# Performance work log

Measured on AMD Instinct MI355X. Metric: run time of the kernel, lower is better.

The kernel has to match this reference:

```python
import jax, jax.numpy as jnp
import numpy as np

RING_SIZES = list(range(3, 27, 2))  # 3,5,...,25 -> 12 rings; (1+12)*96 = 1248
BN_EPS = 1e-5


def _box_sum(x, k):
    """Sum over k x k window (k odd), 'same' zero padding. x: [B,C,H,W].
    O(1) per pixel via summed-area table instead of dense depthwise conv."""
    p = k // 2
    H, W = x.shape[2], x.shape[3]
    xp = jnp.pad(x, ((0, 0), (0, 0), (p, p), (p, p)))
    S = jnp.cumsum(jnp.cumsum(xp, axis=2), axis=3)
    S = jnp.pad(S, ((0, 0), (0, 0), (1, 0), (1, 0)))  # leading zero row/col
    return (S[:, :, k:k + H, k:k + W] - S[:, :, :H, k:k + W]
            - S[:, :, k:k + H, :W] + S[:, :, :H, :W])


def _ring_sum(x, k):
    """Depthwise conv with a k x k ring of ones == box(k) - box(k-2)."""
    inner = x if k == 3 else _box_sum(x, k - 2)
    return _box_sum(x, k) - inner


def _bn_eval(x, gamma, beta, mean, var):
    scale = gamma / jnp.sqrt(var + BN_EPS)
    return x * scale[None, :, None, None] + (beta - mean * scale)[None, :, None, None]


def _conv1x1(x, w, b):
    # x: [B,C,H,W], w: [O,C] -> [B,O,H,W]
    return jnp.einsum('bchw,oc->bohw', x, w) + b[None, :, None, None]


def setup_inputs() -> dict:
    key = jax.random.key(0)
    ks = jax.random.split(key, 13)
    B, C, H, W = 4, 96, 128, 128
    return {
        'x': jax.random.normal(ks[0], (B, C, H, W), jnp.float32),
        'bn1_gamma': jax.random.uniform(ks[1], (1248,), jnp.float32, 0.5, 1.5),
        'bn1_beta': jax.random.normal(ks[2], (1248,), jnp.float32) * 0.1,
        'bn1_mean': jax.random.normal(ks[3], (1248,), jnp.float32),
        'bn1_var': jax.random.uniform(ks[4], (1248,), jnp.float32, 0.5, 1.5),
        'conv1_w': jax.random.normal(ks[5], (512, 1248), jnp.float32) * (1.0 / np.sqrt(1248)),
        'conv1_b': jax.random.normal(ks[6], (512,), jnp.float32) * 0.01,
        'bn2_gamma': jax.random.uniform(ks[7], (512,), jnp.float32, 0.5, 1.5),
        'bn2_beta': jax.random.normal(ks[8], (512,), jnp.float32) * 0.1,
        'bn2_mean': jax.random.normal(ks[9], (512,), jnp.float32),
        'bn2_var': jax.random.uniform(ks[10], (512,), jnp.float32, 0.5, 1.5),
        'conv2_w': jax.random.normal(ks[11], (96, 512), jnp.float32) * (1.0 / np.sqrt(512)),
        'conv2_b': jax.random.normal(ks[12], (96,), jnp.float32) * 0.01,
    }


def reference(x, bn1_gamma, bn1_beta, bn1_mean, bn1_var, conv1_w, conv1_b,
              bn2_gamma, bn2_beta, bn2_mean, bn2_var, conv2_w, conv2_b):
    convs = [x] + [_ring_sum(x, k) for k in RING_SIZES]
    h = jnp.concatenate(convs, axis=1)  # [B, 1248, H, W]
    h = _bn_eval(h, bn1_gamma, bn1_beta, bn1_mean, bn1_var)
    h = jax.nn.relu(_conv1x1(h, conv1_w, conv1_b))
    h = _bn_eval(h, bn2_gamma, bn2_beta, bn2_mean, bn2_var)
    return _conv1x1(h, conv2_w, conv2_b)
```

## Files before the change

### kernel.cpp

```cpp
#include <hip/hip_runtime.h>
#include <hip/hip_bf16.h>
#include <cstdint>

typedef __attribute__((ext_vector_type(8))) short bf16x8;
typedef __attribute__((ext_vector_type(4))) float f32x4;

#define BN_EPS 1e-5f

__global__ __launch_bounds__(256) void prep1_kernel(
    const float* __restrict__ W1, const float* __restrict__ cb1,
    const float* __restrict__ g1, const float* __restrict__ be1,
    const float* __restrict__ mu1, const float* __restrict__ va1,
    __hip_bfloat16* __restrict__ V, float* __restrict__ b1e)
{
  int o = blockIdx.x;
  int t = threadIdx.x;
  const float* wrow = W1 + (size_t)o * 1248;
  float acc = 0.f;
  for (int i = t; i < 1248; i += 256) {
    float s = g1[i] * rsqrtf(va1[i] + BN_EPS);
    float w = wrow[i];
    acc += w * (be1[i] - mu1[i] * s);
    float g = w * s;
    float gn = 0.f;
    if (i < 1152) {
      float sn = g1[i + 96] * rsqrtf(va1[i + 96] + BN_EPS);
      gn = wrow[i + 96] * sn;
    }
    V[(size_t)o * 1248 + i] = __float2bfloat16(g - gn);
  }
  for (int d = 32; d > 0; d >>= 1) acc += __shfl_down(acc, d);
  __shared__ float red[4];
  int lane = t & 63, wv = t >> 6;
  if (lane == 0) red[wv] = acc;
  __syncthreads();
  if (t == 0) b1e[o] = cb1[o] + red[0] + red[1] + red[2] + red[3];
}

__global__ __launch_bounds__(256) void prep2_kernel(
    const float* __restrict__ W2, const float* __restrict__ cb2,
    const float* __restrict__ g2, const float* __restrict__ be2,
    const float* __restrict__ mu2, const float* __restrict__ va2,
    __hip_bfloat16* __restrict__ W2e, float* __restrict__ b2e)
{
  int o = blockIdx.x;
  int t = threadIdx.x;
  const float* wrow = W2 + (size_t)o * 512;
  float acc = 0.f;
  for (int j = t; j < 512; j += 256) {
    float s = g2[j] * rsqrtf(va2[j] + BN_EPS);
    float wv = wrow[j];
    acc += wv * (be2[j] - mu2[j] * s);
    W2e[(size_t)o * 512 + j] = __float2bfloat16(wv * s);
  }
  for (int d = 32; d > 0; d >>= 1) acc += __shfl_down(acc, d);
  __shared__ float red[4];
  int lane = t & 63, wv2 = t >> 6;
  if (lane == 0) red[wv2] = acc;
  __syncthreads();
  if (t == 0) b2e[o] = cb2[o] + red[0] + red[1] + red[2] + red[3];
}

__global__ __launch_bounds__(512) void sat_kernel(
    const float* __restrict__ x, float* __restrict__ SAT)
{
  int plane = blockIdx.x;
  const float* xp = x + (size_t)plane * 16384;
  __shared__ float tile[16384];
  __shared__ float csA[128 * 4];
  __shared__ float csB[128 * 4];
  int t = threadIdx.x;

  for (int i4 = t; i4 < 4096; i4 += 512) {
    int r = i4 >> 5;
    int g = i4 & 31;
    float4 v = *(const float4*)(xp + (size_t)r * 128 + g * 4);
    *(float4*)(tile + r * 128 + ((g ^ (r & 31)) << 2)) = v;
  }
  __syncthreads();

  int r = t & 127, ch = t >> 7;
  {
    float carry = 0.f;
#pragma unroll
    for (int g8 = 0; g8 < 8; ++g8) {
      int g = ch * 8 + g8;
      float* p = tile + r * 128 + ((g ^ (r & 31)) << 2);
      float4 v = *(float4*)p;
      float s0 = carry + v.x, s1 = s0 + v.y, s2 = s1 + v.z, s3 = s2 + v.w;
      float4 o; o.x = s0; o.y = s1; o.z = s2; o.w = s3;
      *(float4*)p = o;
      carry = s3;
    }
    csA[r * 4 + ch] = carry;
  }
  __syncthreads();
  if (ch > 0) {
    float offs = csA[r * 4 + 0];
    if (ch > 1) offs += csA[r * 4 + 1];
    if (ch > 2) offs += csA[r * 4 + 2];
#pragma unroll
    for (int g8 = 0; g8 < 8; ++g8) {
      int g = ch * 8 + g8;
      float* p = tile + r * 128 + ((g ^ (r & 31)) << 2);
      float4 v = *(float4*)p;
      v.x += offs; v.y += offs; v.z += offs; v.w += offs;
      *(float4*)p = v;
    }
  }
  __syncthreads();

  float* Sg = SAT + (size_t)plane * 17028;
  int xcol = t & 127, rc = t >> 7;
  int gc = xcol >> 2, wc = xcol & 3;
  float regs[32];
  {
    float run = 0.f;
#pragma unroll
    for (int r8 = 0; r8 < 32; ++r8) {
      int rr = rc * 32 + r8;
      run += tile[rr * 128 + ((gc ^ (rr & 31)) << 2) + wc];
      regs[r8] = run;
    }
    csB[xcol * 4 + rc] = run;
  }
  if (t < 132) Sg[t] = 0.f;
  if (t < 128) Sg[(t + 1) * 132] = 0.f;
  __syncthreads();

  float offs = 0.f;
  if (rc > 0) offs += csB[xcol * 4 + 0];
  if (rc > 1) offs += csB[xcol * 4 + 1];
  if (rc > 2) offs += csB[xcol * 4 + 2];
#pragma unroll
  for (int r8 = 0; r8 < 32; ++r8) {
    int rr = rc * 32 + r8;
    Sg[(rr + 1) * 132 + xcol + 1] = regs[r8] + offs;
  }
}

__global__ __launch_bounds__(1024) void fused1_kernel(
    const float* __restrict__ SAT, const __hip_bfloat16* __restrict__ V,
    const float* __restrict__ b1e, const __hip_bfloat16* __restrict__ W2e,
    const float* __restrict__ b2e, float* __restrict__ out, int nb, int b0)
{
  extern __shared__ __align__(16) char smem[];
  float* E0 = (float*)smem;
  float* E1 = (float*)(smem + 50688);
  __hip_bfloat16* As0 = (__hip_bfloat16*)(smem + 101376);
  __hip_bfloat16* As1 = (__hip_bfloat16*)(smem + 128000);

  int blk = blockIdx.x;
  int rows_per_xcd = (nb * 128) >> 3;
  int r = (blk & 7) * rows_per_xcd + (blk >> 3);
  int bL = r >> 7, y = r & 127;

  int t = threadIdx.x;
  int lane = t & 63, wv = t >> 6;
  int wm = wv & 1, wn = wv >> 1;
  int lr = lane & 15, quad = lane >> 4;
  int px = t & 127;
  int bg = t >> 7;

  const float* Sb = SAT + (size_t)bL * 96 * 17028;

  f32x4 acc[4][4];
#pragma unroll
  for (int i = 0; i < 4; ++i)
#pragma unroll
    for (int jn = 0; jn < 4; ++jn) acc[i][jn] = (f32x4){0.f, 0.f, 0.f, 0.f};

  auto efill = [&](float* E, int jr) {
    int y1 = (y - jr < 0) ? 0 : (y - jr);
    int y2 = ((y + jr > 127) ? 127 : (y + jr)) + 1;
    for (int idx = t; idx < 3168; idx += 1024) {
      int cl = idx / 33;
      int ck = idx - cl * 33;
      const float* bp = Sb + (size_t)cl * 17028 + ck * 4;
      float4 a = *(const float4*)(bp + y2 * 132);
      float4 b = *(const float4*)(bp + y1 * 132);
      float4 d;
      d.x = a.x - b.x; d.y = a.y - b.y; d.z = a.z - b.z; d.w = a.w - b.w;
      *(float4*)(E + cl * 132 + ck * 4) = d;
    }
  };

  auto build = [&](__hip_bfloat16* As, const float* E, int jr) {
    int x1 = (px - jr < 0) ? 0 : (px - jr);
    int x2 = ((px + jr > 127) ? 127 : (px + jr)) + 1;
    const float* Eb = E + bg * 8 * 132;
    union { bf16x8 v; __hip_bfloat16 h[8]; } pk;
#pragma unroll
    for (int i = 0; i < 8; ++i)
      pk.h[i] = __float2bfloat16(Eb[i * 132 + x2] - Eb[i * 132 + x1]);
    *(bf16x8*)(As + px * 104 + bg * 8) = pk.v;
    if (bg < 4) {
      const float* Eb2 = E + (8 + bg) * 8 * 132;
      union { bf16x8 v; __hip_bfloat16 h[8]; } pk2;
#pragma unroll
      for (int i = 0; i < 8; ++i)
        pk2.h[i] = __float2bfloat16(Eb2[i * 132 + x2] - Eb2[i * 132 + x1]);
      *(bf16x8*)(As + px * 104 + (8 + bg) * 8) = pk2.v;
    }
  };

  auto mfma_ring = [&](int j, const __hip_bfloat16* As) {
    __builtin_amdgcn_s_setprio(1);
#pragma unroll
    for (int sub = 0; sub < 3; ++sub) {
      bf16x8 af[4], bfr[4];
#pragma unroll
      for (int i = 0; i < 4; ++i)
        af[i] = *(const bf16x8*)(As + (wm * 64 + i * 16 + lr) * 104 + sub * 32 + quad * 8);
#pragma unroll
      for (int jn = 0; jn < 4; ++jn)
        bfr[jn] = *(const bf16x8*)(V + (size_t)(wn * 64 + jn * 16 + lr) * 1248
                                   + j * 96 + sub * 32 + quad * 8);
#pragma unroll
      for (int i = 0; i < 4; ++i)
#pragma unroll
        for (int jn = 0; jn < 4; ++jn)
          acc[i][jn] = __builtin_amdgcn_mfma_f32_16x16x32_bf16(af[i], bfr[jn], acc[i][jn], 0, 0, 0);
    }
    __builtin_amdgcn_s_setprio(0);
  };

  auto ring_iter = [&](int j, const float* Esrc, float* Edst,
                       const __hip_bfloat16* Asrc, __hip_bfloat16* Adst) {
    if (wv & 1) {
      mfma_ring(j, Asrc);
      if (j < 11) efill(Edst, j + 2);
      if (j < 12) build(Adst, Esrc, j + 1);
    } else {
      if (j < 11) efill(Edst, j + 2);
      if (j < 12) build(Adst, Esrc, j + 1);
      mfma_ring(j, Asrc);
    }
    __syncthreads();
  };

  efill(E0, 0);
  __syncthreads();
  efill(E1, 1);
  build(As0, E0, 0);
  __syncthreads();

  for (int j = 0; j < 13; j += 2) {
    ring_iter(j, E1, E0, As0, As1);
    if (j + 1 < 13) ring_iter(j + 1, E0, E1, As1, As0);
  }

  __hip_bfloat16* Yst = (__hip_bfloat16*)smem;
#pragma unroll
  for (int jn = 0; jn < 4; ++jn) {
    int n = wn * 64 + jn * 16 + lr;
    float bias = b1e[n];
#pragma unroll
    for (int i = 0; i < 4; ++i) {
#pragma unroll
      for (int rr = 0; rr < 4; ++rr) {
        int m = wm * 64 + i * 16 + quad * 4 + rr;
        float z = acc[i][jn][rr] + bias;
        z = z > 0.f ? z : 0.f;
        Yst[m * 520 + n] = __float2bfloat16(z);
      }
    }
  }
  __syncthreads();

  int pxt = wv & 7;
  int mh = wv >> 3;
  f32x4 acc2[3];
#pragma unroll
  for (int im = 0; im < 3; ++im) acc2[im] = (f32x4){0.f, 0.f, 0.f, 0.f};

  for (int k2 = 0; k2 < 512; k2 += 32) {
    bf16x8 bfr2 = *(const bf16x8*)(Yst + (pxt * 16 + lr) * 520 + k2 + quad * 8);
#pragma unroll
    for (int im = 0; im < 3; ++im) {
      bf16x8 afr2 = *(const bf16x8*)(W2e + (size_t)(mh * 48 + im * 16 + lr) * 512
                                     + k2 + quad * 8);
      acc2[im] = __builtin_amdgcn_mfma_f32_16x16x32_bf16(afr2, bfr2, acc2[im], 0, 0, 0);
    }
  }

  size_t obase = ((size_t)(b0 + bL) * 96) * 16384 + (size_t)y * 128 + pxt * 16 + lr;
#pragma unroll
  for (int im = 0; im < 3; ++im) {
#pragma unroll
    for (int rr = 0; rr < 4; ++rr) {
      int o2 = mh * 48 + im * 16 + quad * 4 + rr;
      out[obase + (size_t)o2 * 16384] = acc2[im][rr] + b2e[o2];
    }
  }
}

extern "C" void kernel_launch(void* const* d_in, const int* in_sizes, int n_in,
                              void* d_out, int out_size, void* d_ws, size_t ws_size,
                              hipStream_t stream)
{
  const float* x   = (const float*)d_in[0];
  const float* g1  = (const float*)d_in[1];
  const float* be1 = (const float*)d_in[2];
  const float* mu1 = (const float*)d_in[3];
  const float* va1 = (const float*)d_in[4];
  const float* W1  = (const float*)d_in[5];
  const float* cb1 = (const float*)d_in[6];
  const float* g2  = (const float*)d_in[7];
  const float* be2 = (const float*)d_in[8];
  const float* mu2 = (const float*)d_in[9];
  const float* va2 = (const float*)d_in[10];
  const float* W2  = (const float*)d_in[11];
  const float* cb2 = (const float*)d_in[12];
  float* out = (float*)d_out;

  hipFuncSetAttribute((const void*)fused1_kernel,
                      hipFuncAttributeMaxDynamicSharedMemorySize, 154624);

  char* w = (char*)d_ws;
  __hip_bfloat16* V   = (__hip_bfloat16*)w; w += (size_t)512 * 1248 * 2;
  __hip_bfloat16* W2e = (__hip_bfloat16*)w; w += (size_t)96 * 512 * 2;
  float* b1e = (float*)w; w += 2048;
  float* b2e = (float*)w; w += 512;
  size_t fixed = (size_t)(w - (char*)d_ws);

  const size_t satB = (size_t)96 * 17028 * 4;
  int nb = (ws_size >= fixed + 4 * satB + 4096) ? 4 : 1;

  float* SAT = (float*)w;

  prep1_kernel<<<512, 256, 0, stream>>>(W1, cb1, g1, be1, mu1, va1, V, b1e);
  prep2_kernel<<<96, 256, 0, stream>>>(W2, cb2, g2, be2, mu2, va2, W2e, b2e);

  for (int b0 = 0; b0 < 4; b0 += nb) {
    sat_kernel<<<nb * 96, 512, 0, stream>>>(x + (size_t)b0 * 96 * 16384, SAT);
    fused1_kernel<<<nb * 128, 1024, 154624, stream>>>(SAT, V, b1e, W2e, b2e, out, nb, b0);
  }
}
```

Before: 302.4 us.

## Restructure fused kernel to 512 threads with larger per-wave tiles and register-staged prefetch

Cuts the fused kernel block from 1024 to 512 threads. Each wave now computes a 128-output by 64-pixel tile with 32 accumulators, taking A fragments from global V and B from shared memory. The double-buffered A tile is replaced by a single buffer, and SAT row differences are prefetched into registers between MFMA sub-steps, with an extra sync per ring. The aim is more register-level reuse of V fragments and better overlap of global loads with MFMA. The cost is much higher register pressure, which makes the launch_bounds(512,2) occupancy target hard to meet, plus an extra barrier per ring iteration.

```diff
diff --git a/kernel.cpp b/kernel.cpp
--- a/kernel.cpp
+++ b/kernel.cpp
@@ -3,6 +3,7 @@
 #include <cstdint>
 
 typedef __attribute__((ext_vector_type(8))) short bf16x8;
+typedef __attribute__((ext_vector_type(4))) short bf16x4;
 typedef __attribute__((ext_vector_type(4))) float f32x4;
 
 #define BN_EPS 1e-5f
@@ -139,7 +140,7 @@
   }
 }
 
-__global__ __launch_bounds__(1024) void fused1_kernel(
+__global__ __launch_bounds__(512, 2) void fused1_kernel(
     const float* __restrict__ SAT, const __hip_bfloat16* __restrict__ V,
     const float* __restrict__ b1e, const __hip_bfloat16* __restrict__ W2e,
     const float* __restrict__ b2e, float* __restrict__ out, int nb, int b0)
@@ -147,8 +148,7 @@
   extern __shared__ __align__(16) char smem[];
   float* E0 = (float*)smem;
   float* E1 = (float*)(smem + 50688);
-  __hip_bfloat16* As0 = (__hip_bfloat16*)(smem + 101376);
-  __hip_bfloat16* As1 = (__hip_bfloat16*)(smem + 128000);
+  __hip_bfloat16* As = (__hip_bfloat16*)(smem + 101376);
 
   int blk = blockIdx.x;
   int rows_per_xcd = (nb * 128) >> 3;
@@ -157,140 +157,163 @@
 
   int t = threadIdx.x;
   int lane = t & 63, wv = t >> 6;
-  int wm = wv & 1, wn = wv >> 1;
+  int wo = wv >> 1, wp = wv & 1;
   int lr = lane & 15, quad = lane >> 4;
   int px = t & 127;
   int bg = t >> 7;
 
   const float* Sb = SAT + (size_t)bL * 96 * 17028;
 
-  f32x4 acc[4][4];
-#pragma unroll
-  for (int i = 0; i < 4; ++i)
-#pragma unroll
-    for (int jn = 0; jn < 4; ++jn) acc[i][jn] = (f32x4){0.f, 0.f, 0.f, 0.f};
-
-  auto efill = [&](float* E, int jr) {
-    int y1 = (y - jr < 0) ? 0 : (y - jr);
-    int y2 = ((y + jr > 127) ? 127 : (y + jr)) + 1;
-    for (int idx = t; idx < 3168; idx += 1024) {
-      int cl = idx / 33;
-      int ck = idx - cl * 33;
+  f32x4 acc[8][4];
+#pragma unroll
+  for (int io = 0; io < 8; ++io)
+#pragma unroll
+    for (int ip = 0; ip < 4; ++ip) acc[io][ip] = (f32x4){0.f, 0.f, 0.f, 0.f};
+
+  float4 ea[3], eb[3];
+  float ta = 0.f, tb = 0.f;
+
+  auto eload = [&](int jr, int h) {
+    int y1 = ((y - jr < 0) ? 0 : (y - jr)) * 132;
+    int y2 = (((y + jr > 127) ? 127 : (y + jr)) + 1) * 132;
+#pragma unroll
+    for (int k = 0; k < 3; ++k) {
+      int idx = t + 512 * (h * 3 + k);
+      int cl = idx >> 5, ck = idx & 31;
       const float* bp = Sb + (size_t)cl * 17028 + ck * 4;
-      float4 a = *(const float4*)(bp + y2 * 132);
-      float4 b = *(const float4*)(bp + y1 * 132);
+      ea[k] = *(const float4*)(bp + y2);
+      eb[k] = *(const float4*)(bp + y1);
+    }
+    if (h == 1 && t < 96) {
+      const float* bp = Sb + (size_t)t * 17028 + 128;
+      ta = bp[y2];
+      tb = bp[y1];
+    }
+  };
+
+  auto ewrite = [&](float* E, int h) {
+#pragma unroll
+    for (int k = 0; k < 3; ++k) {
+      int idx = t + 512 * (h * 3 + k);
+      int cl = idx >> 5, ck = idx & 31;
       float4 d;
-      d.x = a.x - b.x; d.y = a.y - b.y; d.z = a.z - b.z; d.w = a.w - b.w;
+      d.x = ea[k].x - eb[k].x; d.y = ea[k].y - eb[k].y;
+      d.z = ea[k].z - eb[k].z; d.w = ea[k].w - eb[k].w;
       *(float4*)(E + cl * 132 + ck * 4) = d;
     }
+    if (h == 1 && t < 96) E[t * 132 + 128] = ta - tb;
   };
 
-  auto build = [&](__hip_bfloat16* As, const float* E, int jr) {
+  auto build = [&](const float* E, int jr) {
     int x1 = (px - jr < 0) ? 0 : (px - jr);
     int x2 = ((px + jr > 127) ? 127 : (px + jr)) + 1;
-    const float* Eb = E + bg * 8 * 132;
-    union { bf16x8 v; __hip_bfloat16 h[8]; } pk;
-#pragma unroll
-    for (int i = 0; i < 8; ++i)
-      pk.h[i] = __float2bfloat16(Eb[i * 132 + x2] - Eb[i * 132 + x1]);
-    *(bf16x8*)(As + px * 104 + bg * 8) = pk.v;
-    if (bg < 4) {
-      const float* Eb2 = E + (8 + bg) * 8 * 132;
-      union { bf16x8 v; __hip_bfloat16 h[8]; } pk2;
+#pragma unroll
+    for (int k = 0; k < 3; ++k) {
+      int g = bg + 4 * k;
+      const float* Eb = E + g * 8 * 132;
+      union { bf16x8 v; __hip_bfloat16 h[8]; } pk;
 #pragma unroll
       for (int i = 0; i < 8; ++i)
-        pk2.h[i] = __float2bfloat16(Eb2[i * 132 + x2] - Eb2[i * 132 + x1]);
-      *(bf16x8*)(As + px * 104 + (8 + bg) * 8) = pk2.v;
+        pk.h[i] = __float2bfloat16(Eb[i * 132 + x2] - Eb[i * 132 + x1]);
+      *(bf16x8*)(As + px * 104 + g * 8) = pk.v;
     }
   };
 
-  auto mfma_ring = [&](int j, const __hip_bfloat16* As) {
+  auto mfma_sub = [&](int j, int sub) {
+    bf16x8 av[8], bs[4];
+#pragma unroll
+    for (int io = 0; io < 8; ++io)
+      av[io] = *(const bf16x8*)(V + (size_t)(wo * 128 + io * 16 + lr) * 1248
+                                + j * 96 + sub * 32 + quad * 8);
+#pragma unroll
+    for (int ip = 0; ip < 4; ++ip)
+      bs[ip] = *(const bf16x8*)(As + (wp * 64 + ip * 16 + lr) * 104 + sub * 32 + quad * 8);
     __builtin_amdgcn_s_setprio(1);
 #pragma unroll
-    for (int sub = 0; sub < 3; ++sub) {
-      bf16x8 af[4], bfr[4];
-#pragma unroll
-      for (int i = 0; i < 4; ++i)
-        af[i] = *(const bf16x8*)(As + (wm * 64 + i * 16 + lr) * 104 + sub * 32 + quad * 8);
-#pragma unroll
-      for (int jn = 0; jn < 4; ++jn)
-        bfr[jn] = *(const bf16x8*)(V + (size_t)(wn * 64 + jn * 16 + lr) * 1248
-                                   + j * 96 + sub * 32 + quad * 8);
-#pragma unroll
-      for (int i = 0; i < 4; ++i)
-#pragma unroll
-        for (int jn = 0; jn < 4; ++jn)
-          acc[i][jn] = __builtin_amdgcn_mfma_f32_16x16x32_bf16(af[i], bfr[jn], acc[i][jn], 0, 0, 0);
-    }
+    for (int io = 0; io < 8; ++io)
+#pragma unroll
+      for (int ip = 0; ip < 4; ++ip)
+        acc[io][ip] = __builtin_amdgcn_mfma_f32_16x16x32_bf16(av[io], bs[ip], acc[io][ip], 0, 0, 0);
     __builtin_amdgcn_s_setprio(0);
   };
 
-  auto ring_iter = [&](int j, const float* Esrc, float* Edst,
-                       const __hip_bfloat16* Asrc, __hip_bfloat16* Adst) {
-    if (wv & 1) {
-      mfma_ring(j, Asrc);
-      if (j < 11) efill(Edst, j + 2);
-      if (j < 12) build(Adst, Esrc, j + 1);
-    } else {
-      if (j < 11) efill(Edst, j + 2);
-      if (j < 12) build(Adst, Esrc, j + 1);
-      mfma_ring(j, Asrc);
-    }
+  eload(0, 0); ewrite(E0, 0); eload(0, 1); ewrite(E0, 1);
+  __syncthreads();
+  eload(1, 0); ewrite(E1, 0); eload(1, 1);
+  build(E0, 0);
+  ewrite(E1, 1);
+  __syncthreads();
+
+  for (int j = 0; j < 13; ++j) {
+    float* EJ = (j & 1) ? E1 : E0;
+    const float* EK = (j & 1) ? E0 : E1;
+    bool pf = (j < 11);
+    if (pf) eload(j + 2, 0);
+    mfma_sub(j, 0);
+    if (pf) { ewrite(EJ, 0); eload(j + 2, 1); }
+    mfma_sub(j, 1);
+    mfma_sub(j, 2);
+    if (pf) ewrite(EJ, 1);
     __syncthreads();
-  };
-
-  efill(E0, 0);
-  __syncthreads();
-  efill(E1, 1);
-  build(As0, E0, 0);
-  __syncthreads();
-
-  for (int j = 0; j < 13; j += 2) {
-    ring_iter(j, E1, E0, As0, As1);
-    if (j + 1 < 13) ring_iter(j + 1, E0, E1, As1, As0);
+    if (j < 12) build(EK, j + 1);
+    __syncthreads();
   }
 
   __hip_bfloat16* Yst = (__hip_bfloat16*)smem;
 #pragma unroll
-  for (int jn = 0; jn < 4; ++jn) {
-    int n = wn * 64 + jn * 16 + lr;
-    float bias = b1e[n];
-#pragma unroll
-    for (int i = 0; i < 4; ++i) {
+  for (int io = 0; io < 8; ++io) {
+    int o1b = wo * 128 + io * 16 + quad * 4;
+    float4 bias = *(const float4*)(b1e + o1b);
+#pragma unroll
+    for (int ip = 0; ip < 4; ++ip) {
+      int pxx = wp * 64 + ip * 16 + lr;
+      f32x4 a = acc[io][ip];
+      float z0 = a[0] + bias.x; z0 = z0 > 0.f ? z0 : 0.f;
+      float z1 = a[1] + bias.y; z1 = z1 > 0.f ? z1 : 0.f;
+      float z2 = a[2] + bias.z; z2 = z2 > 0.f ? z2 : 0.f;
+      float z3 = a[3] + bias.w; z3 = z3 > 0.f ? z3 : 0.f;
+      union { bf16x4 v; __hip_bfloat16 h[4]; } pk;
+      pk.h[0] = __float2bfloat16(z0); pk.h[1] = __float2bfloat16(z1);
+      pk.h[2] = __float2bfloat16(z2); pk.h[3] = __float2bfloat16(z3);
+      *(bf16x4*)(Yst + pxx * 520 + o1b) = pk.v;
+    }
+  }
+  __syncthreads();
+
+  int og = wv >> 2;
+  int pg = wv & 3;
+  f32x4 acc2[3][2];
+#pragma unroll
+  for (int im = 0; im < 3; ++im)
+#pragma unroll
+    for (int tl = 0; tl < 2; ++tl) acc2[im][tl] = (f32x4){0.f, 0.f, 0.f, 0.f};
+
+  for (int k2 = 0; k2 < 512; k2 += 32) {
+    bf16x8 bfr2[2];
+#pragma unroll
+    for (int tl = 0; tl < 2; ++tl)
+      bfr2[tl] = *(const bf16x8*)(Yst + (pg * 32 + tl * 16 + lr) * 520 + k2 + quad * 8);
+#pragma unroll
+    for (int im = 0; im < 3; ++im) {
+      bf16x8 afr2 = *(const bf16x8*)(W2e + (size_t)(og * 48 + im * 16 + lr) * 512
+                                     + k2 + quad * 8);
+#pragma unroll
+      for (int tl = 0; tl < 2; ++tl)
+        acc2[im][tl] = __builtin_amdgcn_mfma_f32_16x16x32_bf16(afr2, bfr2[tl], acc2[im][tl], 0, 0, 0);
+    }
+  }
+
+  size_t obase = ((size_t)(b0 + bL) * 96) * 16384 + (size_t)y * 128;
+#pragma unroll
+  for (int im = 0; im < 3; ++im) {
+#pragma unroll
+    for (int tl = 0; tl < 2; ++tl) {
+      int pxx = pg * 32 + tl * 16 + lr;
 #pragma unroll
       for (int rr = 0; rr < 4; ++rr) {
-        int m = wm * 64 + i * 16 + quad * 4 + rr;
-        float z = acc[i][jn][rr] + bias;
-        z = z > 0.f ? z : 0.f;
-        Yst[m * 520 + n] = __float2bfloat16(z);
+        int o2 = og * 48 + im * 16 + quad * 4 + rr;
+        out[obase + (size_t)o2 * 16384 + pxx] = acc2[im][tl][rr] + b2e[o2];
       }
-    }
-  }
-  __syncthreads();
-
-  int pxt = wv & 7;
-  int mh = wv >> 3;
-  f32x4 acc2[3];
-#pragma unroll
-  for (int im = 0; im < 3; ++im) acc2[im] = (f32x4){0.f, 0.f, 0.f, 0.f};
-
-  for (int k2 = 0; k2 < 512; k2 += 32) {
-    bf16x8 bfr2 = *(const bf16x8*)(Yst + (pxt * 16 + lr) * 520 + k2 + quad * 8);
-#pragma unroll
-    for (int im = 0; im < 3; ++im) {
-      bf16x8 afr2 = *(const bf16x8*)(W2e + (size_t)(mh * 48 + im * 16 + lr) * 512
-                                     + k2 + quad * 8);
-      acc2[im] = __builtin_amdgcn_mfma_f32_16x16x32_bf16(afr2, bfr2, acc2[im], 0, 0, 0);
-    }
-  }
-
-  size_t obase = ((size_t)(b0 + bL) * 96) * 16384 + (size_t)y * 128 + pxt * 16 + lr;
-#pragma unroll
-  for (int im = 0; im < 3; ++im) {
-#pragma unroll
-    for (int rr = 0; rr < 4; ++rr) {
-      int o2 = mh * 48 + im * 16 + quad * 4 + rr;
-      out[obase + (size_t)o2 * 16384] = acc2[im][rr] + b2e[o2];
     }
   }
 }
@@ -315,7 +338,7 @@
   float* out = (float*)d_out;
 
   hipFuncSetAttribute((const void*)fused1_kernel,
-                      hipFuncAttributeMaxDynamicSharedMemorySize, 154624);
+                      hipFuncAttributeMaxDynamicSharedMemorySize, 133120);
 
   char* w = (char*)d_ws;
   __hip_bfloat16* V   = (__hip_bfloat16*)w; w += (size_t)512 * 1248 * 2;
@@ -334,6 +357,6 @@
 
   for (int b0 = 0; b0 < 4; b0 += nb) {
     sat_kernel<<<nb * 96, 512, 0, stream>>>(x + (size_t)b0 * 96 * 16384, SAT);
-    fused1_kernel<<<nb * 128, 1024, 154624, stream>>>(SAT, V, b1e, W2e, b2e, out, nb, b0);
-  }
-}
+    fused1_kernel<<<nb * 128, 512, 133120, stream>>>(SAT, V, b1e, W2e, b2e, out, nb, b0);
+  }
+}
```

New measurement: 288.9 us. 1.05x faster.

## Split fused kernel into producer/consumer waves over half-row tiles, merge prep kernels

Applied to the files above, without the earlier changes.

Merges the two weight-prep kernels and the SAT kernel into one launch. The main kernel now handles 64-pixel half-rows and uses 1024 blocks. It dedicates half the waves to producing the ring A-tile from the SAT through a small swizzled transposed LDS staging buffer, while the other half run MFMAs, with a double-buffered A tile. Shared memory drops from about 151KB to 65KB, which may let two blocks share a CU. The trade-off is more redundant SAT reads from the halo columns, and only half the waves issue MFMAs.

```diff
diff --git a/kernel.cpp b/kernel.cpp
--- a/kernel.cpp
+++ b/kernel.cpp
@@ -3,73 +3,17 @@
 #include <cstdint>
 
 typedef __attribute__((ext_vector_type(8))) short bf16x8;
+typedef __attribute__((ext_vector_type(4))) short bf16x4;
 typedef __attribute__((ext_vector_type(4))) float f32x4;
 
 #define BN_EPS 1e-5f
 
-__global__ __launch_bounds__(256) void prep1_kernel(
-    const float* __restrict__ W1, const float* __restrict__ cb1,
-    const float* __restrict__ g1, const float* __restrict__ be1,
-    const float* __restrict__ mu1, const float* __restrict__ va1,
-    __hip_bfloat16* __restrict__ V, float* __restrict__ b1e)
-{
-  int o = blockIdx.x;
-  int t = threadIdx.x;
-  const float* wrow = W1 + (size_t)o * 1248;
-  float acc = 0.f;
-  for (int i = t; i < 1248; i += 256) {
-    float s = g1[i] * rsqrtf(va1[i] + BN_EPS);
-    float w = wrow[i];
-    acc += w * (be1[i] - mu1[i] * s);
-    float g = w * s;
-    float gn = 0.f;
-    if (i < 1152) {
-      float sn = g1[i + 96] * rsqrtf(va1[i + 96] + BN_EPS);
-      gn = wrow[i + 96] * sn;
-    }
-    V[(size_t)o * 1248 + i] = __float2bfloat16(g - gn);
-  }
-  for (int d = 32; d > 0; d >>= 1) acc += __shfl_down(acc, d);
-  __shared__ float red[4];
-  int lane = t & 63, wv = t >> 6;
-  if (lane == 0) red[wv] = acc;
-  __syncthreads();
-  if (t == 0) b1e[o] = cb1[o] + red[0] + red[1] + red[2] + red[3];
-}
-
-__global__ __launch_bounds__(256) void prep2_kernel(
-    const float* __restrict__ W2, const float* __restrict__ cb2,
-    const float* __restrict__ g2, const float* __restrict__ be2,
-    const float* __restrict__ mu2, const float* __restrict__ va2,
-    __hip_bfloat16* __restrict__ W2e, float* __restrict__ b2e)
-{
-  int o = blockIdx.x;
-  int t = threadIdx.x;
-  const float* wrow = W2 + (size_t)o * 512;
-  float acc = 0.f;
-  for (int j = t; j < 512; j += 256) {
-    float s = g2[j] * rsqrtf(va2[j] + BN_EPS);
-    float wv = wrow[j];
-    acc += wv * (be2[j] - mu2[j] * s);
-    W2e[(size_t)o * 512 + j] = __float2bfloat16(wv * s);
-  }
-  for (int d = 32; d > 0; d >>= 1) acc += __shfl_down(acc, d);
-  __shared__ float red[4];
-  int lane = t & 63, wv2 = t >> 6;
-  if (lane == 0) red[wv2] = acc;
-  __syncthreads();
-  if (t == 0) b2e[o] = cb2[o] + red[0] + red[1] + red[2] + red[3];
-}
-
-__global__ __launch_bounds__(512) void sat_kernel(
-    const float* __restrict__ x, float* __restrict__ SAT)
-{
-  int plane = blockIdx.x;
-  const float* xp = x + (size_t)plane * 16384;
+__device__ __forceinline__ void sat_plane(const float* __restrict__ xp,
+                                          float* __restrict__ Sg, int t)
+{
   __shared__ float tile[16384];
-  __shared__ float csA[128 * 4];
-  __shared__ float csB[128 * 4];
-  int t = threadIdx.x;
+  __shared__ float csA[512];
+  __shared__ float csB[512];
 
   for (int i4 = t; i4 < 4096; i4 += 512) {
     int r = i4 >> 5;
@@ -110,7 +54,6 @@
   }
   __syncthreads();
 
-  float* Sg = SAT + (size_t)plane * 17028;
   int xcol = t & 127, rc = t >> 7;
   int gc = xcol >> 2, wc = xcol & 3;
   float regs[32];
@@ -126,6 +69,10 @@
   }
   if (t < 132) Sg[t] = 0.f;
   if (t < 128) Sg[(t + 1) * 132] = 0.f;
+  if (t < 128) {
+    float* rp = Sg + (size_t)(t + 1) * 132;
+    rp[129] = 0.f; rp[130] = 0.f; rp[131] = 0.f;
+  }
   __syncthreads();
 
   float offs = 0.f;
@@ -139,158 +86,246 @@
   }
 }
 
-__global__ __launch_bounds__(1024) void fused1_kernel(
+__global__ __launch_bounds__(512) void prepsat_kernel(
+    const float* __restrict__ W1, const float* __restrict__ cb1,
+    const float* __restrict__ g1, const float* __restrict__ be1,
+    const float* __restrict__ mu1, const float* __restrict__ va1,
+    const float* __restrict__ W2, const float* __restrict__ cb2,
+    const float* __restrict__ g2, const float* __restrict__ be2,
+    const float* __restrict__ mu2, const float* __restrict__ va2,
+    const float* __restrict__ x,
+    __hip_bfloat16* __restrict__ V, float* __restrict__ b1e,
+    __hip_bfloat16* __restrict__ W2e, float* __restrict__ b2e,
+    float* __restrict__ SAT, int nplanes)
+{
+  int blk = blockIdx.x;
+  int t = threadIdx.x;
+  if (blk < 512) {
+    __shared__ float red[8];
+    int o = blk;
+    const float* wrow = W1 + (size_t)o * 1248;
+    float acc = 0.f;
+    for (int i = t; i < 1248; i += 512) {
+      float s = g1[i] * rsqrtf(va1[i] + BN_EPS);
+      float w = wrow[i];
+      acc += w * (be1[i] - mu1[i] * s);
+      float g = w * s;
+      float gn = 0.f;
+      if (i < 1152) {
+        float sn = g1[i + 96] * rsqrtf(va1[i + 96] + BN_EPS);
+        gn = wrow[i + 96] * sn;
+      }
+      V[(size_t)o * 1248 + i] = __float2bfloat16(g - gn);
+    }
+    for (int d = 32; d > 0; d >>= 1) acc += __shfl_down(acc, d);
+    int lane = t & 63, wvv = t >> 6;
+    if (lane == 0) red[wvv] = acc;
+    __syncthreads();
+    if (t == 0) {
+      float s = cb1[o];
+#pragma unroll
+      for (int i = 0; i < 8; ++i) s += red[i];
+      b1e[o] = s;
+    }
+  } else if (blk < 608) {
+    __shared__ float red2[8];
+    int o = blk - 512;
+    const float* wrow = W2 + (size_t)o * 512;
+    float acc = 0.f;
+    {
+      int j = t;
+      float s = g2[j] * rsqrtf(va2[j] + BN_EPS);
+      float wv = wrow[j];
+      acc = wv * (be2[j] - mu2[j] * s);
+      W2e[(size_t)o * 512 + j] = __float2bfloat16(wv * s);
+    }
+    for (int d = 32; d > 0; d >>= 1) acc += __shfl_down(acc, d);
+    int lane = t & 63, wvv = t >> 6;
+    if (lane == 0) red2[wvv] = acc;
+    __syncthreads();
+    if (t == 0) {
+      float s = cb2[o];
+#pragma unroll
+      for (int i = 0; i < 8; ++i) s += red2[i];
+      b2e[o] = s;
+    }
+  } else {
+    int plane = blk - 608;
+    if (plane < nplanes)
+      sat_plane(x + (size_t)plane * 16384, SAT + (size_t)plane * 17028, t);
+  }
+}
+
+__global__ __launch_bounds__(512) void satonly_kernel(
+    const float* __restrict__ x, float* __restrict__ SAT)
+{
+  sat_plane(x + (size_t)blockIdx.x * 16384,
+            SAT + (size_t)blockIdx.x * 17028, threadIdx.x);
+}
+
+__global__ __launch_bounds__(1024) void fused3_kernel(
     const float* __restrict__ SAT, const __hip_bfloat16* __restrict__ V,
     const float* __restrict__ b1e, const __hip_bfloat16* __restrict__ W2e,
     const float* __restrict__ b2e, float* __restrict__ out, int nb, int b0)
 {
   extern __shared__ __align__(16) char smem[];
-  float* E0 = (float*)smem;
-  float* E1 = (float*)(smem + 50688);
-  __hip_bfloat16* As0 = (__hip_bfloat16*)(smem + 101376);
-  __hip_bfloat16* As1 = (__hip_bfloat16*)(smem + 128000);
+  float* ET = (float*)smem;
+  __hip_bfloat16* As0 = (__hip_bfloat16*)(smem + 36800);
+  __hip_bfloat16* As1 = (__hip_bfloat16*)(smem + 50112);
 
   int blk = blockIdx.x;
-  int rows_per_xcd = (nb * 128) >> 3;
-  int r = (blk & 7) * rows_per_xcd + (blk >> 3);
-  int bL = r >> 7, y = r & 127;
+  int per_xcd = (nb * 256) >> 3;
+  int r = (blk & 7) * per_xcd + (blk >> 3);
+  int bL = r >> 8;
+  int rem = r & 255;
+  int y = rem >> 1, h = rem & 1;
+  int x0 = h * 64 - 12;
+  const float* Sb = SAT + (size_t)bL * 96 * 17028;
 
   int t = threadIdx.x;
   int lane = t & 63, wv = t >> 6;
-  int wm = wv & 1, wn = wv >> 1;
   int lr = lane & 15, quad = lane >> 4;
-  int px = t & 127;
-  int bg = t >> 7;
-
-  const float* Sb = SAT + (size_t)bL * 96 * 17028;
+  bool isC = (wv & 4) != 0;
+  int role = (wv & 3) | (((wv >> 3) & 1) << 2);
 
   f32x4 acc[4][4];
 #pragma unroll
-  for (int i = 0; i < 4; ++i)
-#pragma unroll
-    for (int jn = 0; jn < 4; ++jn) acc[i][jn] = (f32x4){0.f, 0.f, 0.f, 0.f};
-
-  auto efill = [&](float* E, int jr) {
-    int y1 = (y - jr < 0) ? 0 : (y - jr);
-    int y2 = ((y + jr > 127) ? 127 : (y + jr)) + 1;
-    for (int idx = t; idx < 3168; idx += 1024) {
-      int cl = idx / 33;
-      int ck = idx - cl * 33;
-      const float* bp = Sb + (size_t)cl * 17028 + ck * 4;
-      float4 a = *(const float4*)(bp + y2 * 132);
-      float4 b = *(const float4*)(bp + y1 * 132);
-      float4 d;
-      d.x = a.x - b.x; d.y = a.y - b.y; d.z = a.z - b.z; d.w = a.w - b.w;
-      *(float4*)(E + cl * 132 + ck * 4) = d;
+  for (int io = 0; io < 4; ++io)
+#pragma unroll
+    for (int ip = 0; ip < 4; ++ip) acc[io][ip] = (f32x4){0.f, 0.f, 0.f, 0.f};
+
+  int cb = role * 12;
+  int pxl = lane;
+  int pxg = h * 64 + pxl;
+
+  auto produce = [&](__hip_bfloat16* As, int jr) {
+    int y1 = (y - jr < 0 ? 0 : y - jr) * 132;
+    int y2 = ((y + jr > 127 ? 127 : y + jr) + 1) * 132;
+#pragma unroll
+    for (int it = 0; it < 5; ++it) {
+      int idx = lane + (it << 6);
+      if (idx < 276) {
+        int clp = idx / 46;
+        int xq = idx - clp * 46;
+        int cl = cb + clp * 2;
+        int xg = x0 + (xq << 1);
+        xg = xg < 0 ? 0 : (xg > 128 ? 128 : xg);
+        const float* p0 = Sb + (size_t)cl * 17028 + xg;
+        float2 a2 = *(const float2*)(p0 + y2);
+        float2 a1 = *(const float2*)(p0 + y1);
+        float2 c2 = *(const float2*)(p0 + 17028 + y2);
+        float2 c1 = *(const float2*)(p0 + 17028 + y1);
+        int xl = xq << 1;
+        int sw = ((xl >> 3) & 7) << 2;
+        int cw = cl ^ sw;
+        *(float2*)(ET + xl * 100 + cw) = make_float2(a2.x - a1.x, c2.x - c1.x);
+        *(float2*)(ET + xl * 100 + 100 + cw) = make_float2(a2.y - a1.y, c2.y - c1.y);
+      }
+    }
+    asm volatile("s_waitcnt lgkmcnt(0)" ::: "memory");
+    __builtin_amdgcn_sched_barrier(0);
+    int x2l = ((pxg + jr > 127 ? 127 : pxg + jr) + 1) - x0;
+    int x1l = ((pxg - jr < 0 ? 0 : pxg - jr)) - x0;
+    int s2 = ((x2l >> 3) & 7) << 2;
+    int s1 = ((x1l >> 3) & 7) << 2;
+    const float* r2 = ET + x2l * 100;
+    const float* r1 = ET + x1l * 100;
+#pragma unroll
+    for (int k = 0; k < 3; ++k) {
+      int c = cb + (k << 2);
+      float4 e2 = *(const float4*)(r2 + (c ^ s2));
+      float4 e1 = *(const float4*)(r1 + (c ^ s1));
+      union { bf16x4 v; __hip_bfloat16 hh[4]; } pk;
+      pk.hh[0] = __float2bfloat16(e2.x - e1.x);
+      pk.hh[1] = __float2bfloat16(e2.y - e1.y);
+      pk.hh[2] = __float2bfloat16(e2.z - e1.z);
+      pk.hh[3] = __float2bfloat16(e2.w - e1.w);
+      *(bf16x4*)(As + pxl * 104 + c) = pk.v;
     }
   };
 
-  auto build = [&](__hip_bfloat16* As, const float* E, int jr) {
-    int x1 = (px - jr < 0) ? 0 : (px - jr);
-    int x2 = ((px + jr > 127) ? 127 : (px + jr)) + 1;
-    const float* Eb = E + bg * 8 * 132;
-    union { bf16x8 v; __hip_bfloat16 h[8]; } pk;
-#pragma unroll
-    for (int i = 0; i < 8; ++i)
-      pk.h[i] = __float2bfloat16(Eb[i * 132 + x2] - Eb[i * 132 + x1]);
-    *(bf16x8*)(As + px * 104 + bg * 8) = pk.v;
-    if (bg < 4) {
-      const float* Eb2 = E + (8 + bg) * 8 * 132;
-      union { bf16x8 v; __hip_bfloat16 h[8]; } pk2;
-#pragma unroll
-      for (int i = 0; i < 8; ++i)
-        pk2.h[i] = __float2bfloat16(Eb2[i * 132 + x2] - Eb2[i * 132 + x1]);
-      *(bf16x8*)(As + px * 104 + (8 + bg) * 8) = pk2.v;
+  const __hip_bfloat16* Vb = V + (size_t)(role * 64) * 1248;
+  auto mfma_ring = [&](int j, const __hip_bfloat16* As) {
+#pragma unroll
+    for (int sub = 0; sub < 3; ++sub) {
+      bf16x8 av[4], bs[4];
+#pragma unroll
+      for (int io = 0; io < 4; ++io)
+        av[io] = *(const bf16x8*)(Vb + (size_t)(io * 16 + lr) * 1248
+                                  + j * 96 + sub * 32 + quad * 8);
+#pragma unroll
+      for (int ip = 0; ip < 4; ++ip)
+        bs[ip] = *(const bf16x8*)(As + (ip * 16 + lr) * 104 + sub * 32 + quad * 8);
+      __builtin_amdgcn_s_setprio(1);
+#pragma unroll
+      for (int io = 0; io < 4; ++io)
+#pragma unroll
+        for (int ip = 0; ip < 4; ++ip)
+          acc[io][ip] = __builtin_amdgcn_mfma_f32_16x16x32_bf16(
+              av[io], bs[ip], acc[io][ip], 0, 0, 0);
+      __builtin_amdgcn_s_setprio(0);
     }
   };
 
-  auto mfma_ring = [&](int j, const __hip_bfloat16* As) {
-    __builtin_amdgcn_s_setprio(1);
-#pragma unroll
-    for (int sub = 0; sub < 3; ++sub) {
-      bf16x8 af[4], bfr[4];
-#pragma unroll
-      for (int i = 0; i < 4; ++i)
-        af[i] = *(const bf16x8*)(As + (wm * 64 + i * 16 + lr) * 104 + sub * 32 + quad * 8);
-#pragma unroll
-      for (int jn = 0; jn < 4; ++jn)
-        bfr[jn] = *(const bf16x8*)(V + (size_t)(wn * 64 + jn * 16 + lr) * 1248
-                                   + j * 96 + sub * 32 + quad * 8);
-#pragma unroll
-      for (int i = 0; i < 4; ++i)
-#pragma unroll
-        for (int jn = 0; jn < 4; ++jn)
-          acc[i][jn] = __builtin_amdgcn_mfma_f32_16x16x32_bf16(af[i], bfr[jn], acc[i][jn], 0, 0, 0);
-    }
-    __builtin_amdgcn_s_setprio(0);
-  };
-
-  auto ring_iter = [&](int j, const float* Esrc, float* Edst,
-                       const __hip_bfloat16* Asrc, __hip_bfloat16* Adst) {
-    if (wv & 1) {
-      mfma_ring(j, Asrc);
-      if (j < 11) efill(Edst, j + 2);
-      if (j < 12) build(Adst, Esrc, j + 1);
+  if (!isC) produce(As0, 0);
+  __syncthreads();
+
+  for (int j = 0; j < 13; ++j) {
+    if (!isC) {
+      if (j < 12) produce((j & 1) ? As0 : As1, j + 1);
     } else {
-      if (j < 11) efill(Edst, j + 2);
-      if (j < 12) build(Adst, Esrc, j + 1);
-      mfma_ring(j, Asrc);
+      mfma_ring(j, (j & 1) ? As1 : As0);
     }
     __syncthreads();
-  };
-
-  efill(E0, 0);
-  __syncthreads();
-  efill(E1, 1);
-  build(As0, E0, 0);
-  __syncthreads();
-
-  for (int j = 0; j < 13; j += 2) {
-    ring_iter(j, E1, E0, As0, As1);
-    if (j + 1 < 13) ring_iter(j + 1, E0, E1, As1, As0);
   }
 
   __hip_bfloat16* Yst = (__hip_bfloat16*)smem;
-#pragma unroll
-  for (int jn = 0; jn < 4; ++jn) {
-    int n = wn * 64 + jn * 16 + lr;
-    float bias = b1e[n];
-#pragma unroll
-    for (int i = 0; i < 4; ++i) {
+  if (isC) {
+#pragma unroll
+    for (int io = 0; io < 4; ++io) {
+      int o1b = role * 64 + io * 16 + quad * 4;
+      float4 bias = *(const float4*)(b1e + o1b);
+#pragma unroll
+      for (int ip = 0; ip < 4; ++ip) {
+        int pxx = ip * 16 + lr;
+        f32x4 a = acc[io][ip];
+        float z0 = a[0] + bias.x; z0 = z0 > 0.f ? z0 : 0.f;
+        float z1 = a[1] + bias.y; z1 = z1 > 0.f ? z1 : 0.f;
+        float z2 = a[2] + bias.z; z2 = z2 > 0.f ? z2 : 0.f;
+        float z3 = a[3] + bias.w; z3 = z3 > 0.f ? z3 : 0.f;
+        union { bf16x4 v; __hip_bfloat16 hh[4]; } pk;
+        pk.hh[0] = __float2bfloat16(z0); pk.hh[1] = __float2bfloat16(z1);
+        pk.hh[2] = __float2bfloat16(z2); pk.hh[3] = __float2bfloat16(z3);
+        *(bf16x4*)(Yst + pxx * 520 + o1b) = pk.v;
+      }
+    }
+  }
+  __syncthreads();
+
+  if (isC) {
+    int mh = role >> 2;
+    int pq = role & 3;
+    f32x4 acc2[3];
+#pragma unroll
+    for (int im = 0; im < 3; ++im) acc2[im] = (f32x4){0.f, 0.f, 0.f, 0.f};
+    for (int k2 = 0; k2 < 512; k2 += 32) {
+      bf16x8 b2f = *(const bf16x8*)(Yst + (pq * 16 + lr) * 520 + k2 + quad * 8);
+#pragma unroll
+      for (int im = 0; im < 3; ++im) {
+        bf16x8 a2f = *(const bf16x8*)(W2e + (size_t)(mh * 48 + im * 16 + lr) * 512
+                                      + k2 + quad * 8);
+        acc2[im] = __builtin_amdgcn_mfma_f32_16x16x32_bf16(a2f, b2f, acc2[im], 0, 0, 0);
+      }
+    }
+    size_t obase = ((size_t)(b0 + bL) * 96) * 16384 + (size_t)y * 128
+                   + h * 64 + pq * 16 + lr;
+#pragma unroll
+    for (int im = 0; im < 3; ++im) {
 #pragma unroll
       for (int rr = 0; rr < 4; ++rr) {
-        int m = wm * 64 + i * 16 + quad * 4 + rr;
-        float z = acc[i][jn][rr] + bias;
-        z = z > 0.f ? z : 0.f;
-        Yst[m * 520 + n] = __float2bfloat16(z);
-      }
-    }
-  }
-  __syncthreads();
-
-  int pxt = wv & 7;
-  int mh = wv >> 3;
-  f32x4 acc2[3];
-#pragma unroll
-  for (int im = 0; im < 3; ++im) acc2[im] = (f32x4){0.f, 0.f, 0.f, 0.f};
-
-  for (int k2 = 0; k2 < 512; k2 += 32) {
-    bf16x8 bfr2 = *(const bf16x8*)(Yst + (pxt * 16 + lr) * 520 + k2 + quad * 8);
-#pragma unroll
-    for (int im = 0; im < 3; ++im) {
-      bf16x8 afr2 = *(const bf16x8*)(W2e + (size_t)(mh * 48 + im * 16 + lr) * 512
-                                     + k2 + quad * 8);
-      acc2[im] = __builtin_amdgcn_mfma_f32_16x16x32_bf16(afr2, bfr2, acc2[im], 0, 0, 0);
-    }
-  }
-
-  size_t obase = ((size_t)(b0 + bL) * 96) * 16384 + (size_t)y * 128 + pxt * 16 + lr;
-#pragma unroll
-  for (int im = 0; im < 3; ++im) {
-#pragma unroll
-    for (int rr = 0; rr < 4; ++rr) {
-      int o2 = mh * 48 + im * 16 + quad * 4 + rr;
-      out[obase + (size_t)o2 * 16384] = acc2[im][rr] + b2e[o2];
+        int o2 = mh * 48 + im * 16 + quad * 4 + rr;
+        out[obase + (size_t)o2 * 16384] = acc2[im][rr] + b2e[o2];
+      }
     }
   }
 }
@@ -314,8 +349,8 @@
   const float* cb2 = (const float*)d_in[12];
   float* out = (float*)d_out;
 
-  hipFuncSetAttribute((const void*)fused1_kernel,
-                      hipFuncAttributeMaxDynamicSharedMemorySize, 154624);
+  hipFuncSetAttribute((const void*)fused3_kernel,
+                      hipFuncAttributeMaxDynamicSharedMemorySize, 66560);
 
   char* w = (char*)d_ws;
   __hip_bfloat16* V   = (__hip_bfloat16*)w; w += (size_t)512 * 1248 * 2;
@@ -329,11 +364,18 @@
 
   float* SAT = (float*)w;
 
-  prep1_kernel<<<512, 256, 0, stream>>>(W1, cb1, g1, be1, mu1, va1, V, b1e);
-  prep2_kernel<<<96, 256, 0, stream>>>(W2, cb2, g2, be2, mu2, va2, W2e, b2e);
-
-  for (int b0 = 0; b0 < 4; b0 += nb) {
-    sat_kernel<<<nb * 96, 512, 0, stream>>>(x + (size_t)b0 * 96 * 16384, SAT);
-    fused1_kernel<<<nb * 128, 1024, 154624, stream>>>(SAT, V, b1e, W2e, b2e, out, nb, b0);
-  }
-}
+  if (nb == 4) {
+    prepsat_kernel<<<992, 512, 0, stream>>>(W1, cb1, g1, be1, mu1, va1,
+                                            W2, cb2, g2, be2, mu2, va2,
+                                            x, V, b1e, W2e, b2e, SAT, 384);
+    fused3_kernel<<<1024, 1024, 66560, stream>>>(SAT, V, b1e, W2e, b2e, out, 4, 0);
+  } else {
+    prepsat_kernel<<<608, 512, 0, stream>>>(W1, cb1, g1, be1, mu1, va1,
+                                            W2, cb2, g2, be2, mu2, va2,
+                                            x, V, b1e, W2e, b2e, SAT, 0);
+    for (int b0 = 0; b0 < 4; ++b0) {
+      satonly_kernel<<<96, 512, 0, stream>>>(x + (size_t)b0 * 96 * 16384, SAT);
+      fused3_kernel<<<256, 1024, 66560, stream>>>(SAT, V, b1e, W2e, b2e, out, 1, b0);
+    }
+  }
+}
```

After: 398.7 us. +31.8%, slower.
